# Kernel tuning notes

Measured on AMD Instinct MI355X. Metric: run time of the kernel, lower is better.

## Reference

```python
import jax, jax.numpy as jnp
import numpy as np

NUM_GROUPS = 16   # static upper bound on group ids (actual ids in [0, 12))
MIN_COUNT = 10    # min_subgroup_count


def setup_inputs() -> dict:
    key = jax.random.key(0)
    ks = jax.random.split(key, 7)
    B = 32768
    N = 16777216  # dataset_size
    probs = jax.random.uniform(ks[0], (B,), dtype=jnp.float32)
    labels = jax.random.randint(ks[1], (B,), 0, 2, dtype=jnp.int32)
    groups = jax.random.randint(ks[2], (B,), 0, 12, dtype=jnp.int32)
    indices = jax.random.randint(ks[3], (B,), 0, N, dtype=jnp.int32)
    # persistent buffers, pre-filled with valid mid-epoch state
    score_buffer = jax.random.uniform(ks[4], (N,), dtype=jnp.float32)
    label_buffer = jax.random.randint(ks[5], (N,), 0, 2, dtype=jnp.int32)
    group_buffer = jax.random.randint(ks[6], (N,), 0, 12, dtype=jnp.int32)
    return {"probs": probs, "labels": labels, "groups": groups, "indices": indices,
            "score_buffer": score_buffer, "label_buffer": label_buffer,
            "group_buffer": group_buffer}


def reference(probs, labels, groups, indices, score_buffer, label_buffer, group_buffer):
    # scatter current batch into dataset-sized buffers (functional clone + write)
    scores = score_buffer.at[indices].set(probs)
    labs = label_buffer.at[indices].set(labels)
    grps = group_buffer.at[indices].set(groups)

    valid = (~jnp.isnan(scores)) & (labs >= 0) & (grps >= 0)
    scores = jnp.where(valid, scores, 0.0)        # kill NaNs before weighted sums
    seg = jnp.where(valid, grps, 0)               # invalid rows get weight 0 anyway

    def group_var(lab_val):
        # per-group mean of scores restricted to (valid & label==lab_val),
        # then unbiased variance across groups meeting the min-count threshold
        w = (valid & (labs == lab_val)).astype(scores.dtype)
        sums = jax.ops.segment_sum(scores * w, seg, num_segments=NUM_GROUPS)
        cnts = jax.ops.segment_sum(w, seg, num_segments=NUM_GROUPS)
        avg = sums / jnp.maximum(cnts, 1.0)
        incl = (cnts >= MIN_COUNT).astype(scores.dtype)
        n = incl.sum()
        mean = (avg * incl).sum() / jnp.maximum(n, 1.0)
        var = (incl * (avg - mean) ** 2).sum() / jnp.maximum(n - 1.0, 1.0)  # ddof=1
        return var, n

    pos_var, n_pos = group_var(1)
    neg_var, n_neg = group_var(0)
    pos_ok = n_pos >= 2.0
    neg_ok = n_neg >= 2.0
    loss = jnp.where(pos_ok & neg_ok, 0.5 * (pos_var + neg_var),
                     jnp.where(pos_ok, pos_var,
                               jnp.where(neg_ok, neg_var, 0.0)))
    return loss
```

## Files before the change

kernel.cpp:

```cpp
#include <hip/hip_runtime.h>
#include <hip/hip_bf16.h>


#define TBL   65536u
#define TBLM  (TBL - 1u)
#define NGR   12
#define NBK   24
#define NCOL  25
#define NTHR  256
#define CHUNK 16384
#define ITER  (CHUNK / 4 / NTHR)
#define DEPTH 4
#define MINC  10.0

__device__ __forceinline__ unsigned hash_idx(unsigned idx) {
    return (idx * 2654435761u) & TBLM;
}

__global__ void k_vote(const int* __restrict__ indices,
                       unsigned long long* __restrict__ table,
                       unsigned* __restrict__ bitmap, int B) {
    int b = blockIdx.x * blockDim.x + threadIdx.x;
    if (b >= B) return;
    unsigned idx = (unsigned)indices[b];
    atomicOr(&bitmap[idx >> 5], 1u << (idx & 31u));
    unsigned long long key = ((unsigned long long)(idx + 1u)) << 32;
    unsigned long long val = key | (unsigned long long)(unsigned)b;
    unsigned slot = hash_idx(idx);
    for (;;) {
        unsigned long long prev = atomicCAS(&table[slot], 0ULL, val);
        if (prev == 0ULL) return;
        if ((prev >> 32) == (unsigned long long)(idx + 1u)) {
            atomicMax(&table[slot], val);
            return;
        }
        slot = (slot + 1u) & TBLM;
    }
}

__global__ void k_resolve(const unsigned long long* __restrict__ table,
                          const float* __restrict__ probs,
                          const int* __restrict__ labels,
                          const int* __restrict__ groups,
                          float4* __restrict__ tbl2) {
    int s = blockIdx.x * blockDim.x + threadIdx.x;
    unsigned long long e = table[s];
    unsigned hi = (unsigned)(e >> 32);
    float4 r = make_float4(0.f, 0.f, 0.f, 0.f);
    if (hi) {
        int b = (int)(e & 0xffffffffu);
        r.x = probs[b];
        r.y = __int_as_float(labels[b]);
        r.z = __int_as_float(groups[b]);
        r.w = __uint_as_float(hi);
    }
    tbl2[s] = r;
}

__device__ __forceinline__ void apply_ovr(int idx, float& s, int& l, int& g,
        const float4* __restrict__ tbl2) {
    unsigned slot = hash_idx((unsigned)idx);
    unsigned hi = (unsigned)idx + 1u;
    for (;;) {
        float4 r = tbl2[slot];
        if (__float_as_uint(r.w) == hi) {
            s = r.x; l = __float_as_int(r.y); g = __float_as_int(r.z);
            return;
        }
        slot = (slot + 1u) & TBLM;
    }
}

__device__ __forceinline__ void quad_p1(float* __restrict__ row,
        float4 s4, int4 l4, int4 g4, unsigned bits, int v,
        const float4* __restrict__ tbl2) {
    float ss[4] = {s4.x, s4.y, s4.z, s4.w};
    int   ll[4] = {l4.x, l4.y, l4.z, l4.w};
    int   gg[4] = {g4.x, g4.y, g4.z, g4.w};
    float val[4]; int bkt[4];
#pragma unroll
    for (int e = 0; e < 4; ++e) {
        float s = ss[e]; int l = ll[e], g = gg[e];
        if ((bits >> e) & 1u)
            apply_ovr((v << 2) + e, s, l, g, tbl2);
        bool valid = (s == s) && ((unsigned)l < 2u) && ((unsigned)g < (unsigned)NGR);
        bkt[e] = valid ? (g * 2 + l) : NBK;
        val[e] = valid ? s : 0.f;
    }
#define MRG(i, j) { bool m_ = (bkt[i] == bkt[j]); \
                    val[i] += m_ ? val[j] : 0.f;  \
                    bkt[j] = m_ ? NBK : bkt[j];   \
                    val[j] = m_ ? 0.f : val[j]; }
    MRG(0,1) MRG(0,2) MRG(0,3) MRG(1,2) MRG(1,3) MRG(2,3)
#undef MRG
    float a0 = row[bkt[0]], a1 = row[bkt[1]], a2 = row[bkt[2]], a3 = row[bkt[3]];
    row[bkt[0]] = a0 + val[0];
    row[bkt[1]] = a1 + val[1];
    row[bkt[2]] = a2 + val[2];
    row[bkt[3]] = a3 + val[3];
}

__global__ __launch_bounds__(NTHR) void k_pass1(
        const float* __restrict__ sb, const int* __restrict__ lb,
        const int* __restrict__ gb, const unsigned* __restrict__ bitmap,
        const float4* __restrict__ tbl2,
        float* __restrict__ bsum, int n, int nblk) {
    __shared__ float s_acc[NTHR * NCOL];
    int tid = threadIdx.x, blk = blockIdx.x;
    for (int i = tid; i < NTHR * NCOL; i += NTHR) s_acc[i] = 0.f;
    __syncthreads();
    float* row = &s_acc[tid * NCOL];
    int vbase = (blk * CHUNK) >> 2, nv = n >> 2;
    if (vbase + (CHUNK >> 2) <= nv) {
        int v0 = vbase + tid;
        float4 ps[DEPTH]; int4 pl[DEPTH], pg[DEPTH]; unsigned pb[DEPTH];
#pragma unroll
        for (int d = 0; d < DEPTH; ++d) {
            int v = v0 + d * NTHR;
            ps[d] = ((const float4*)sb)[v];
            pl[d] = ((const int4*)lb)[v];
            pg[d] = ((const int4*)gb)[v];
            pb[d] = bitmap[v >> 3];
        }
        unsigned sh = (unsigned)((v0 & 7) * 4);
#pragma unroll
        for (int it = 0; it < ITER; ++it) {
            int d = it & (DEPTH - 1);
            int v = v0 + it * NTHR;
            float4 s4 = ps[d]; int4 l4 = pl[d], g4 = pg[d];
            unsigned bits = pb[d] >> sh;
            if (it + DEPTH < ITER) {
                int w = v + DEPTH * NTHR;
                ps[d] = ((const float4*)sb)[w];
                pl[d] = ((const int4*)lb)[w];
                pg[d] = ((const int4*)gb)[w];
                pb[d] = bitmap[w >> 3];
            }
            asm volatile("" ::: "memory");
            quad_p1(row, s4, l4, g4, bits, v, tbl2);
        }
    } else {
        for (int it = 0; it < ITER; ++it) {
            int v = vbase + it * NTHR + tid;
            if (v >= nv) break;
            float4 s4 = ((const float4*)sb)[v];
            int4   l4 = ((const int4*)lb)[v];
            int4   g4 = ((const int4*)gb)[v];
            unsigned bits = bitmap[v >> 3] >> ((v & 7) * 4);
            quad_p1(row, s4, l4, g4, bits, v, tbl2);
        }
    }
    if (blk == nblk - 1) {
        for (int i = (nv << 2) + tid; i < n; i += NTHR) {
            float s = sb[i]; int l = lb[i], g = gb[i];
            if ((bitmap[i >> 5] >> (i & 31)) & 1u)
                apply_ovr(i, s, l, g, tbl2);
            bool valid = (s == s) && ((unsigned)l < 2u) && ((unsigned)g < (unsigned)NGR);
            int bk = valid ? (g * 2 + l) : NBK;
            row[bk] += valid ? s : 0.f;
        }
    }
    __syncthreads();
    if (tid < NBK * 8) {
        int bkt = tid >> 3, sub = tid & 7;
        float sm = 0.f;
        for (int j = 0; j < 32; ++j) sm += s_acc[(sub * 32 + j) * NCOL + bkt];
        for (int d = 4; d >= 1; d >>= 1) sm += __shfl_down(sm, d, 8);
        if (!sub) bsum[bkt * nblk + blk] = sm;
    }
}

__global__ void k_scan(const float* __restrict__ bsum,
                       float* __restrict__ bpref, int nblk) {
    __shared__ double sc[NTHR];
    int t = threadIdx.x, k = blockIdx.x;
    const float* src = bsum  + (size_t)k * nblk;
    float*       dst = bpref + (size_t)k * nblk;
    double carry = 0.0;
    for (int s0 = 0; s0 < nblk; s0 += 4 * NTHR) {
        int i0 = s0 + 4 * t;
        float x0 = (i0 + 0 < nblk) ? src[i0 + 0] : 0.f;
        float x1 = (i0 + 1 < nblk) ? src[i0 + 1] : 0.f;
        float x2 = (i0 + 2 < nblk) ? src[i0 + 2] : 0.f;
        float x3 = (i0 + 3 < nblk) ? src[i0 + 3] : 0.f;
        double p0 = (double)x0, p1 = p0 + x1, p2 = p1 + x2, tot = p2 + x3;
        sc[t] = tot;
        __syncthreads();
        for (int st = 1; st < NTHR; st <<= 1) {
            double a = (t >= st) ? sc[t - st] : 0.0;
            __syncthreads();
            sc[t] += a;
            __syncthreads();
        }
        double excl = carry + sc[t] - tot;
        if (i0 + 0 < nblk) dst[i0 + 0] = (float)excl;
        if (i0 + 1 < nblk) dst[i0 + 1] = (float)(excl + p0);
        if (i0 + 2 < nblk) dst[i0 + 2] = (float)(excl + p1);
        if (i0 + 3 < nblk) dst[i0 + 3] = (float)(excl + p2);
        double bt = sc[NTHR - 1];
        __syncthreads();
        carry += bt;
    }
}

__device__ __forceinline__ double aload_d(const double* p) {
    unsigned long long u = __hip_atomic_load((const unsigned long long*)p,
                              __ATOMIC_RELAXED, __HIP_MEMORY_SCOPE_AGENT);
    return __longlong_as_double((long long)u);
}

__device__ __forceinline__ void quad_p2(float2* __restrict__ row,
        const float2* __restrict__ s_model,
        float4 s4, int4 l4, int4 g4, unsigned bits, int v, int base,
        const float4* __restrict__ tbl2) {
    float ss[4] = {s4.x, s4.y, s4.z, s4.w};
    int   ll[4] = {l4.x, l4.y, l4.z, l4.w};
    int   gg[4] = {g4.x, g4.y, g4.z, g4.w};
    float cv[4], cn[4]; int bkt[4];
#pragma unroll
    for (int e = 0; e < 4; ++e) {
        int idx = (v << 2) + e;
        float s = ss[e]; int l = ll[e], g = gg[e];
        if ((bits >> e) & 1u)
            apply_ovr(idx, s, l, g, tbl2);
        bool valid = (s == s) && ((unsigned)l < 2u) && ((unsigned)g < (unsigned)NGR);
        int bk = valid ? (g * 2 + l) : NBK;
        float2 m = s_model[bk];
        float S = fmaf(m.y, (float)(idx - base), m.x);
        float T = S + s;
        unsigned ue = __float_as_uint(T) & 0x7f800000u;
        float c;
        if (ue < (24u << 23)) c = s;
        else {
            unsigned ub = ue - (23u << 23);
            float u    = __uint_as_float(ub);
            float uinv = __uint_as_float((254u << 23) - ub);
            c = u * rintf(s * uinv);
        }
        bkt[e] = bk;
        cv[e] = valid ? c : 0.f;
        cn[e] = valid ? 1.f : 0.f;
    }
#define MRG(i, j) { bool m_ = (bkt[i] == bkt[j]); \
                    cv[i] += m_ ? cv[j] : 0.f;    \
                    cn[i] += m_ ? cn[j] : 0.f;    \
                    bkt[j] = m_ ? NBK : bkt[j];   \
                    cv[j] = m_ ? 0.f : cv[j];     \
                    cn[j] = m_ ? 0.f : cn[j]; }
    MRG(0,1) MRG(0,2) MRG(0,3) MRG(1,2) MRG(1,3) MRG(2,3)
#undef MRG
    float2 a0 = row[bkt[0]], a1 = row[bkt[1]], a2 = row[bkt[2]], a3 = row[bkt[3]];
    a0.x += cv[0]; a0.y += cn[0];
    a1.x += cv[1]; a1.y += cn[1];
    a2.x += cv[2]; a2.y += cn[2];
    a3.x += cv[3]; a3.y += cn[3];
    row[bkt[0]] = a0; row[bkt[1]] = a1; row[bkt[2]] = a2; row[bkt[3]] = a3;
}

__global__ __launch_bounds__(NTHR) void k_pass2(
        const float* __restrict__ sb, const int* __restrict__ lb,
        const int* __restrict__ gb, const unsigned* __restrict__ bitmap,
        const float4* __restrict__ tbl2,
        const float* __restrict__ bsum, const float* __restrict__ bpref,
        double* __restrict__ acc_sum, double* __restrict__ acc_cnt,
        unsigned* __restrict__ done, float* __restrict__ out,
        int n, int nblk) {
    __shared__ float2 s_acc[NTHR * NCOL];
    __shared__ float2 s_model[NCOL];
    int tid = threadIdx.x, blk = blockIdx.x;
    for (int i = tid; i < NTHR * NCOL; i += NTHR) s_acc[i] = make_float2(0.f, 0.f);
    if (tid < NBK)
        s_model[tid] = make_float2(bpref[tid * nblk + blk],
                                   bsum[tid * nblk + blk] * (1.0f / CHUNK));
    if (tid == NBK) s_model[NBK] = make_float2(0.f, 0.f);
    __syncthreads();
    float2* row = &s_acc[tid * NCOL];
    int base = blk * CHUNK;
    int vbase = base >> 2, nv = n >> 2;
    if (vbase + (CHUNK >> 2) <= nv) {
        int v0 = vbase + tid;
        float4 ps[DEPTH]; int4 pl[DEPTH], pg[DEPTH]; unsigned pb[DEPTH];
#pragma unroll
        for (int d = 0; d < DEPTH; ++d) {
            int v = v0 + d * NTHR;
            ps[d] = ((const float4*)sb)[v];
            pl[d] = ((const int4*)lb)[v];
            pg[d] = ((const int4*)gb)[v];
            pb[d] = bitmap[v >> 3];
        }
        unsigned sh = (unsigned)((v0 & 7) * 4);
#pragma unroll
        for (int it = 0; it < ITER; ++it) {
            int d = it & (DEPTH - 1);
            int v = v0 + it * NTHR;
            float4 s4 = ps[d]; int4 l4 = pl[d], g4 = pg[d];
            unsigned bits = pb[d] >> sh;
            if (it + DEPTH < ITER) {
                int w = v + DEPTH * NTHR;
                ps[d] = ((const float4*)sb)[w];
                pl[d] = ((const int4*)lb)[w];
                pg[d] = ((const int4*)gb)[w];
                pb[d] = bitmap[w >> 3];
            }
            asm volatile("" ::: "memory");
            quad_p2(row, s_model, s4, l4, g4, bits, v, base, tbl2);
        }
    } else {
        for (int it = 0; it < ITER; ++it) {
            int v = vbase + it * NTHR + tid;
            if (v >= nv) break;
            float4 s4 = ((const float4*)sb)[v];
            int4   l4 = ((const int4*)lb)[v];
            int4   g4 = ((const int4*)gb)[v];
            unsigned bits = bitmap[v >> 3] >> ((v & 7) * 4);
            quad_p2(row, s_model, s4, l4, g4, bits, v, base, tbl2);
        }
    }
    if (blk == nblk - 1) {
        for (int i = (nv << 2) + tid; i < n; i += NTHR) {
            float s = sb[i]; int l = lb[i], g = gb[i];
            if ((bitmap[i >> 5] >> (i & 31)) & 1u)
                apply_ovr(i, s, l, g, tbl2);
            bool valid = (s == s) && ((unsigned)l < 2u) && ((unsigned)g < (unsigned)NGR);
            int bk = valid ? (g * 2 + l) : NBK;
            float2 m = s_model[bk];
            float S = fmaf(m.y, (float)(i - base), m.x);
            float T = S + s;
            unsigned ue = __float_as_uint(T) & 0x7f800000u;
            float c;
            if (ue < (24u << 23)) c = s;
            else {
                unsigned ub = ue - (23u << 23);
                float u    = __uint_as_float(ub);
                float uinv = __uint_as_float((254u << 23) - ub);
                c = u * rintf(s * uinv);
            }
            float2 a = row[bk];
            a.x += valid ? c : 0.f;
            a.y += valid ? 1.f : 0.f;
            row[bk] = a;
        }
    }
    __syncthreads();
    if (tid < NBK * 8) {
        int bkt = tid >> 3, sub = tid & 7;
        float sm = 0.f, cc = 0.f;
        for (int j = 0; j < 32; ++j) {
            float2 a = s_acc[(sub * 32 + j) * NCOL + bkt];
            sm += a.x; cc += a.y;
        }
        for (int d = 4; d >= 1; d >>= 1) {
            sm += __shfl_down(sm, d, 8);
            cc += __shfl_down(cc, d, 8);
        }
        if (!sub) {
            atomicAdd(&acc_sum[bkt], (double)sm);
            atomicAdd(&acc_cnt[bkt], (double)cc);
        }
    }
    __syncthreads();
    if (tid == 0) {
        __threadfence();
        unsigned r = __hip_atomic_fetch_add(done, 1u, __ATOMIC_ACQ_REL,
                                            __HIP_MEMORY_SCOPE_AGENT);
        if (r == (unsigned)(gridDim.x - 1)) {
            double var[2], nn[2];
            for (int l = 0; l < 2; ++l) {
                double avg[NGR];
                double ncnt = 0.0, s = 0.0;
                for (int g = 0; g < NGR; ++g) {
                    double c  = aload_d(&acc_cnt[g * 2 + l]);
                    double sm = aload_d(&acc_sum[g * 2 + l]);
                    double a = sm / fmax(c, 1.0);
                    avg[g] = a;
                    if (c >= MINC) { ncnt += 1.0; s += a; }
                }
                double mean = s / fmax(ncnt, 1.0), v = 0.0;
                for (int g = 0; g < NGR; ++g) {
                    double c = aload_d(&acc_cnt[g * 2 + l]);
                    if (c >= MINC) { double d = avg[g] - mean; v += d * d; }
                }
                var[l] = v / fmax(ncnt - 1.0, 1.0);
                nn[l] = ncnt;
            }
            bool p = nn[1] >= 2.0, q = nn[0] >= 2.0;
            double loss = (p && q) ? 0.5 * (var[1] + var[0])
                        : (p ? var[1] : (q ? var[0] : 0.0));
            out[0] = (float)loss;
        }
    }
}

extern "C" void kernel_launch(void* const* d_in, const int* in_sizes, int n_in,
                              void* d_out, int out_size, void* d_ws, size_t ws_size,
                              hipStream_t stream) {
    const float* probs   = (const float*)d_in[0];
    const int*   labels  = (const int*)d_in[1];
    const int*   groups  = (const int*)d_in[2];
    const int*   indices = (const int*)d_in[3];
    const float* sb      = (const float*)d_in[4];
    const int*   lb      = (const int*)d_in[5];
    const int*   gb      = (const int*)d_in[6];
    int B = in_sizes[0];
    int n = in_sizes[4];
    int nblk   = (n + CHUNK - 1) / CHUNK;
    int nwords = (n + 31) / 32;

    char* ws = (char*)d_ws;
    size_t off = 0;
    unsigned long long* table = (unsigned long long*)(ws + off); off += (size_t)TBL * 8;
    unsigned* bitmap  = (unsigned*)(ws + off); off += (size_t)nwords * 4;
    double*   acc_sum = (double*)(ws + off);   off += NBK * 8;
    double*   acc_cnt = (double*)(ws + off);   off += NBK * 8;
    unsigned* done    = (unsigned*)(ws + off); off += 8;
    size_t zero_bytes = off;
    float4*   tbl2    = (float4*)(ws + off);   off += (size_t)TBL * 16;
    float*    bsum    = (float*)(ws + off);    off += (size_t)nblk * NBK * 4;
    float*    bpref   = (float*)(ws + off);    off += (size_t)nblk * NBK * 4;

    hipMemsetAsync(d_ws, 0, zero_bytes, stream);

    dim3 bblk((B + NTHR - 1) / NTHR);
    hipLaunchKernelGGL(k_vote, bblk, dim3(NTHR), 0, stream,
                       indices, table, bitmap, B);
    hipLaunchKernelGGL(k_resolve, dim3(TBL / NTHR), dim3(NTHR), 0, stream,
                       table, probs, labels, groups, tbl2);
    hipLaunchKernelGGL(k_pass1, dim3(nblk), dim3(NTHR), 0, stream,
                       sb, lb, gb, bitmap, tbl2, bsum, n, nblk);
    hipLaunchKernelGGL(k_scan, dim3(NBK), dim3(NTHR), 0, stream,
                       bsum, bpref, nblk);
    hipLaunchKernelGGL(k_pass2, dim3(nblk), dim3(NTHR), 0, stream,
                       sb, lb, gb, bitmap, tbl2, bsum, bpref,
                       acc_sum, acc_cnt, done, (float*)d_out, n, nblk);
}
```

Measured before the change: 334.7 us.

## Fuse prefix scan into pass1 tail and move counts from pass2 to pass1

```diff
diff --git a/kernel.cpp b/kernel.cpp
--- a/kernel.cpp
+++ b/kernel.cpp
@@ -8,9 +8,11 @@
 #define NBK   24
 #define NCOL  25
 #define NTHR  256
+#define NW    (NTHR / 64)
 #define CHUNK 16384
 #define ITER  (CHUNK / 4 / NTHR)
 #define DEPTH 4
+#define GRP   4
 #define MINC  10.0
 
 __device__ __forceinline__ unsigned hash_idx(unsigned idx) {
@@ -71,26 +73,49 @@
     }
 }
 
+__device__ __forceinline__ float aload_f(const float* p) {
+    unsigned u = __hip_atomic_load((const unsigned*)p,
+                     __ATOMIC_RELAXED, __HIP_MEMORY_SCOPE_AGENT);
+    return __uint_as_float(u);
+}
+__device__ __forceinline__ void astore_f(float* p, float v) {
+    __hip_atomic_store((unsigned*)p, __float_as_uint(v),
+                       __ATOMIC_RELAXED, __HIP_MEMORY_SCOPE_AGENT);
+}
+__device__ __forceinline__ double aload_d(const double* p) {
+    unsigned long long u = __hip_atomic_load((const unsigned long long*)p,
+                              __ATOMIC_RELAXED, __HIP_MEMORY_SCOPE_AGENT);
+    return __longlong_as_double((long long)u);
+}
+
 __device__ __forceinline__ void quad_p1(float* __restrict__ row,
+        unsigned* __restrict__ cntw,
         float4 s4, int4 l4, int4 g4, unsigned bits, int v,
         const float4* __restrict__ tbl2) {
     float ss[4] = {s4.x, s4.y, s4.z, s4.w};
     int   ll[4] = {l4.x, l4.y, l4.z, l4.w};
     int   gg[4] = {g4.x, g4.y, g4.z, g4.w};
-    float val[4]; int bkt[4];
+    if (bits & 0xFu) {
+#pragma unroll
+        for (int e = 0; e < 4; ++e)
+            if ((bits >> e) & 1u)
+                apply_ovr((v << 2) + e, ss[e], ll[e], gg[e], tbl2);
+    }
+    float val[4]; int bkt[4], cn[4];
 #pragma unroll
     for (int e = 0; e < 4; ++e) {
-        float s = ss[e]; int l = ll[e], g = gg[e];
-        if ((bits >> e) & 1u)
-            apply_ovr((v << 2) + e, s, l, g, tbl2);
-        bool valid = (s == s) && ((unsigned)l < 2u) && ((unsigned)g < (unsigned)NGR);
-        bkt[e] = valid ? (g * 2 + l) : NBK;
-        val[e] = valid ? s : 0.f;
+        bool valid = (ss[e] == ss[e]) && ((unsigned)ll[e] < 2u) &&
+                     ((unsigned)gg[e] < (unsigned)NGR);
+        bkt[e] = valid ? (gg[e] * 2 + ll[e]) : NBK;
+        val[e] = valid ? ss[e] : 0.f;
+        cn[e]  = valid ? 1 : 0;
     }
 #define MRG(i, j) { bool m_ = (bkt[i] == bkt[j]); \
                     val[i] += m_ ? val[j] : 0.f;  \
+                    cn[i]  += m_ ? cn[j] : 0;     \
                     bkt[j] = m_ ? NBK : bkt[j];   \
-                    val[j] = m_ ? 0.f : val[j]; }
+                    val[j] = m_ ? 0.f : val[j];   \
+                    cn[j]  = m_ ? 0 : cn[j]; }
     MRG(0,1) MRG(0,2) MRG(0,3) MRG(1,2) MRG(1,3) MRG(2,3)
 #undef MRG
     float a0 = row[bkt[0]], a1 = row[bkt[1]], a2 = row[bkt[2]], a3 = row[bkt[3]];
@@ -98,18 +123,32 @@
     row[bkt[1]] = a1 + val[1];
     row[bkt[2]] = a2 + val[2];
     row[bkt[3]] = a3 + val[3];
+    atomicAdd(&cntw[bkt[0]], (unsigned)cn[0]);
+    atomicAdd(&cntw[bkt[1]], (unsigned)cn[1]);
+    atomicAdd(&cntw[bkt[2]], (unsigned)cn[2]);
+    atomicAdd(&cntw[bkt[3]], (unsigned)cn[3]);
 }
 
 __global__ __launch_bounds__(NTHR) void k_pass1(
         const float* __restrict__ sb, const int* __restrict__ lb,
         const int* __restrict__ gb, const unsigned* __restrict__ bitmap,
         const float4* __restrict__ tbl2,
-        float* __restrict__ bsum, int n, int nblk) {
-    __shared__ float s_acc[NTHR * NCOL];
+        float* __restrict__ bsum, float* __restrict__ bpref,
+        double* __restrict__ acc_cnt, unsigned* __restrict__ done1,
+        int n, int nblk) {
+    __shared__ __align__(16) float s_acc[NTHR * NCOL];
+    __shared__ unsigned s_cnt[NW * NCOL];
+    __shared__ unsigned s_last;
     int tid = threadIdx.x, blk = blockIdx.x;
     for (int i = tid; i < NTHR * NCOL; i += NTHR) s_acc[i] = 0.f;
-    __syncthreads();
+    if (tid < NW * NCOL) s_cnt[tid] = 0u;
+    __syncthreads();
+    int wv = tid >> 6;
+    if (wv == 1) __builtin_amdgcn_s_sleep(4);
+    else if (wv == 2) __builtin_amdgcn_s_sleep(7);
+    else if (wv == 3) __builtin_amdgcn_s_sleep(10);
     float* row = &s_acc[tid * NCOL];
+    unsigned* cntw = &s_cnt[wv * NCOL];
     int vbase = (blk * CHUNK) >> 2, nv = n >> 2;
     if (vbase + (CHUNK >> 2) <= nv) {
         int v0 = vbase + tid;
@@ -137,7 +176,7 @@
                 pb[d] = bitmap[w >> 3];
             }
             asm volatile("" ::: "memory");
-            quad_p1(row, s4, l4, g4, bits, v, tbl2);
+            quad_p1(row, cntw, s4, l4, g4, bits, v, tbl2);
         }
     } else {
         for (int it = 0; it < ITER; ++it) {
@@ -147,7 +186,7 @@
             int4   l4 = ((const int4*)lb)[v];
             int4   g4 = ((const int4*)gb)[v];
             unsigned bits = bitmap[v >> 3] >> ((v & 7) * 4);
-            quad_p1(row, s4, l4, g4, bits, v, tbl2);
+            quad_p1(row, cntw, s4, l4, g4, bits, v, tbl2);
         }
     }
     if (blk == nblk - 1) {
@@ -158,6 +197,7 @@
             bool valid = (s == s) && ((unsigned)l < 2u) && ((unsigned)g < (unsigned)NGR);
             int bk = valid ? (g * 2 + l) : NBK;
             row[bk] += valid ? s : 0.f;
+            atomicAdd(&cntw[bk], valid ? 1u : 0u);
         }
     }
     __syncthreads();
@@ -166,65 +206,90 @@
         float sm = 0.f;
         for (int j = 0; j < 32; ++j) sm += s_acc[(sub * 32 + j) * NCOL + bkt];
         for (int d = 4; d >= 1; d >>= 1) sm += __shfl_down(sm, d, 8);
-        if (!sub) bsum[bkt * nblk + blk] = sm;
-    }
-}
-
-__global__ void k_scan(const float* __restrict__ bsum,
-                       float* __restrict__ bpref, int nblk) {
-    __shared__ double sc[NTHR];
-    int t = threadIdx.x, k = blockIdx.x;
-    const float* src = bsum  + (size_t)k * nblk;
-    float*       dst = bpref + (size_t)k * nblk;
-    double carry = 0.0;
-    for (int s0 = 0; s0 < nblk; s0 += 4 * NTHR) {
-        int i0 = s0 + 4 * t;
-        float x0 = (i0 + 0 < nblk) ? src[i0 + 0] : 0.f;
-        float x1 = (i0 + 1 < nblk) ? src[i0 + 1] : 0.f;
-        float x2 = (i0 + 2 < nblk) ? src[i0 + 2] : 0.f;
-        float x3 = (i0 + 3 < nblk) ? src[i0 + 3] : 0.f;
-        double p0 = (double)x0, p1 = p0 + x1, p2 = p1 + x2, tot = p2 + x3;
-        sc[t] = tot;
-        __syncthreads();
-        for (int st = 1; st < NTHR; st <<= 1) {
-            double a = (t >= st) ? sc[t - st] : 0.0;
+        if (!sub) astore_f(&bsum[bkt * nblk + blk], sm);
+    }
+    if (tid < NBK) {
+        unsigned tot = 0;
+#pragma unroll
+        for (int w = 0; w < NW; ++w) tot += s_cnt[w * NCOL + tid];
+        if (tot) atomicAdd(&acc_cnt[tid], (double)tot);
+    }
+    __syncthreads();
+    if (tid == 0) {
+        __threadfence();
+        unsigned r = __hip_atomic_fetch_add(done1, 1u, __ATOMIC_ACQ_REL,
+                                            __HIP_MEMORY_SCOPE_AGENT);
+        s_last = (r == (unsigned)(gridDim.x - 1)) ? 1u : 0u;
+    }
+    __syncthreads();
+    if (!s_last) return;
+    double* sc2 = (double*)s_acc;
+    int t = tid;
+    for (int k0 = 0; k0 < NBK; k0 += GRP) {
+        double carry[GRP];
+#pragma unroll
+        for (int q = 0; q < GRP; ++q) carry[q] = 0.0;
+        for (int s0 = 0; s0 < nblk; s0 += 4 * NTHR) {
+            int i0 = s0 + 4 * t;
+            double p0[GRP], p1[GRP], p2[GRP], tt[GRP];
+#pragma unroll
+            for (int q = 0; q < GRP; ++q) {
+                const float* src = bsum + (size_t)(k0 + q) * nblk;
+                float x0 = (i0 + 0 < nblk) ? aload_f(src + i0 + 0) : 0.f;
+                float x1 = (i0 + 1 < nblk) ? aload_f(src + i0 + 1) : 0.f;
+                float x2 = (i0 + 2 < nblk) ? aload_f(src + i0 + 2) : 0.f;
+                float x3 = (i0 + 3 < nblk) ? aload_f(src + i0 + 3) : 0.f;
+                p0[q] = (double)x0; p1[q] = p0[q] + x1;
+                p2[q] = p1[q] + x2; tt[q] = p2[q] + x3;
+                sc2[q * NTHR + t] = tt[q];
+            }
             __syncthreads();
-            sc[t] += a;
+            for (int st = 1; st < NTHR; st <<= 1) {
+                double a[GRP];
+#pragma unroll
+                for (int q = 0; q < GRP; ++q)
+                    a[q] = (t >= st) ? sc2[q * NTHR + t - st] : 0.0;
+                __syncthreads();
+#pragma unroll
+                for (int q = 0; q < GRP; ++q) sc2[q * NTHR + t] += a[q];
+                __syncthreads();
+            }
+#pragma unroll
+            for (int q = 0; q < GRP; ++q) {
+                double excl = carry[q] + sc2[q * NTHR + t] - tt[q];
+                float* dst = bpref + (size_t)(k0 + q) * nblk;
+                if (i0 + 0 < nblk) dst[i0 + 0] = (float)excl;
+                if (i0 + 1 < nblk) dst[i0 + 1] = (float)(excl + p0[q]);
+                if (i0 + 2 < nblk) dst[i0 + 2] = (float)(excl + p1[q]);
+                if (i0 + 3 < nblk) dst[i0 + 3] = (float)(excl + p2[q]);
+                carry[q] += sc2[q * NTHR + NTHR - 1];
+            }
             __syncthreads();
         }
-        double excl = carry + sc[t] - tot;
-        if (i0 + 0 < nblk) dst[i0 + 0] = (float)excl;
-        if (i0 + 1 < nblk) dst[i0 + 1] = (float)(excl + p0);
-        if (i0 + 2 < nblk) dst[i0 + 2] = (float)(excl + p1);
-        if (i0 + 3 < nblk) dst[i0 + 3] = (float)(excl + p2);
-        double bt = sc[NTHR - 1];
-        __syncthreads();
-        carry += bt;
-    }
-}
-
-__device__ __forceinline__ double aload_d(const double* p) {
-    unsigned long long u = __hip_atomic_load((const unsigned long long*)p,
-                              __ATOMIC_RELAXED, __HIP_MEMORY_SCOPE_AGENT);
-    return __longlong_as_double((long long)u);
-}
-
-__device__ __forceinline__ void quad_p2(float2* __restrict__ row,
+    }
+}
+
+__device__ __forceinline__ void quad_p2(float* __restrict__ row,
         const float2* __restrict__ s_model,
         float4 s4, int4 l4, int4 g4, unsigned bits, int v, int base,
         const float4* __restrict__ tbl2) {
     float ss[4] = {s4.x, s4.y, s4.z, s4.w};
     int   ll[4] = {l4.x, l4.y, l4.z, l4.w};
     int   gg[4] = {g4.x, g4.y, g4.z, g4.w};
-    float cv[4], cn[4]; int bkt[4];
+    if (bits & 0xFu) {
+#pragma unroll
+        for (int e = 0; e < 4; ++e)
+            if ((bits >> e) & 1u)
+                apply_ovr((v << 2) + e, ss[e], ll[e], gg[e], tbl2);
+    }
+    float cv[4]; int bkt[4];
 #pragma unroll
     for (int e = 0; e < 4; ++e) {
         int idx = (v << 2) + e;
-        float s = ss[e]; int l = ll[e], g = gg[e];
-        if ((bits >> e) & 1u)
-            apply_ovr(idx, s, l, g, tbl2);
-        bool valid = (s == s) && ((unsigned)l < 2u) && ((unsigned)g < (unsigned)NGR);
-        int bk = valid ? (g * 2 + l) : NBK;
+        float s = ss[e];
+        bool valid = (s == s) && ((unsigned)ll[e] < 2u) &&
+                     ((unsigned)gg[e] < (unsigned)NGR);
+        int bk = valid ? (gg[e] * 2 + ll[e]) : NBK;
         float2 m = s_model[bk];
         float S = fmaf(m.y, (float)(idx - base), m.x);
         float T = S + s;
@@ -239,22 +304,18 @@
         }
         bkt[e] = bk;
         cv[e] = valid ? c : 0.f;
-        cn[e] = valid ? 1.f : 0.f;
     }
 #define MRG(i, j) { bool m_ = (bkt[i] == bkt[j]); \
                     cv[i] += m_ ? cv[j] : 0.f;    \
-                    cn[i] += m_ ? cn[j] : 0.f;    \
                     bkt[j] = m_ ? NBK : bkt[j];   \
-                    cv[j] = m_ ? 0.f : cv[j];     \
-                    cn[j] = m_ ? 0.f : cn[j]; }
+                    cv[j] = m_ ? 0.f : cv[j]; }
     MRG(0,1) MRG(0,2) MRG(0,3) MRG(1,2) MRG(1,3) MRG(2,3)
 #undef MRG
-    float2 a0 = row[bkt[0]], a1 = row[bkt[1]], a2 = row[bkt[2]], a3 = row[bkt[3]];
-    a0.x += cv[0]; a0.y += cn[0];
-    a1.x += cv[1]; a1.y += cn[1];
-    a2.x += cv[2]; a2.y += cn[2];
-    a3.x += cv[3]; a3.y += cn[3];
-    row[bkt[0]] = a0; row[bkt[1]] = a1; row[bkt[2]] = a2; row[bkt[3]] = a3;
+    float a0 = row[bkt[0]], a1 = row[bkt[1]], a2 = row[bkt[2]], a3 = row[bkt[3]];
+    row[bkt[0]] = a0 + cv[0];
+    row[bkt[1]] = a1 + cv[1];
+    row[bkt[2]] = a2 + cv[2];
+    row[bkt[3]] = a3 + cv[3];
 }
 
 __global__ __launch_bounds__(NTHR) void k_pass2(
@@ -263,18 +324,22 @@
         const float4* __restrict__ tbl2,
         const float* __restrict__ bsum, const float* __restrict__ bpref,
         double* __restrict__ acc_sum, double* __restrict__ acc_cnt,
-        unsigned* __restrict__ done, float* __restrict__ out,
+        unsigned* __restrict__ done2, float* __restrict__ out,
         int n, int nblk) {
-    __shared__ float2 s_acc[NTHR * NCOL];
+    __shared__ float s_acc[NTHR * NCOL];
     __shared__ float2 s_model[NCOL];
     int tid = threadIdx.x, blk = blockIdx.x;
-    for (int i = tid; i < NTHR * NCOL; i += NTHR) s_acc[i] = make_float2(0.f, 0.f);
+    for (int i = tid; i < NTHR * NCOL; i += NTHR) s_acc[i] = 0.f;
     if (tid < NBK)
         s_model[tid] = make_float2(bpref[tid * nblk + blk],
                                    bsum[tid * nblk + blk] * (1.0f / CHUNK));
     if (tid == NBK) s_model[NBK] = make_float2(0.f, 0.f);
     __syncthreads();
-    float2* row = &s_acc[tid * NCOL];
+    int wv = tid >> 6;
+    if (wv == 1) __builtin_amdgcn_s_sleep(4);
+    else if (wv == 2) __builtin_amdgcn_s_sleep(7);
+    else if (wv == 3) __builtin_amdgcn_s_sleep(10);
+    float* row = &s_acc[tid * NCOL];
     int base = blk * CHUNK;
     int vbase = base >> 2, nv = n >> 2;
     if (vbase + (CHUNK >> 2) <= nv) {
@@ -335,33 +400,21 @@
                 float uinv = __uint_as_float((254u << 23) - ub);
                 c = u * rintf(s * uinv);
             }
-            float2 a = row[bk];
-            a.x += valid ? c : 0.f;
-            a.y += valid ? 1.f : 0.f;
-            row[bk] = a;
+            row[bk] += valid ? c : 0.f;
         }
     }
     __syncthreads();
     if (tid < NBK * 8) {
         int bkt = tid >> 3, sub = tid & 7;
-        float sm = 0.f, cc = 0.f;
-        for (int j = 0; j < 32; ++j) {
-            float2 a = s_acc[(sub * 32 + j) * NCOL + bkt];
-            sm += a.x; cc += a.y;
-        }
-        for (int d = 4; d >= 1; d >>= 1) {
-            sm += __shfl_down(sm, d, 8);
-            cc += __shfl_down(cc, d, 8);
-        }
-        if (!sub) {
-            atomicAdd(&acc_sum[bkt], (double)sm);
-            atomicAdd(&acc_cnt[bkt], (double)cc);
-        }
+        float sm = 0.f;
+        for (int j = 0; j < 32; ++j) sm += s_acc[(sub * 32 + j) * NCOL + bkt];
+        for (int d = 4; d >= 1; d >>= 1) sm += __shfl_down(sm, d, 8);
+        if (!sub) atomicAdd(&acc_sum[bkt], (double)sm);
     }
     __syncthreads();
     if (tid == 0) {
         __threadfence();
-        unsigned r = __hip_atomic_fetch_add(done, 1u, __ATOMIC_ACQ_REL,
+        unsigned r = __hip_atomic_fetch_add(done2, 1u, __ATOMIC_ACQ_REL,
                                             __HIP_MEMORY_SCOPE_AGENT);
         if (r == (unsigned)(gridDim.x - 1)) {
             double var[2], nn[2];
@@ -410,9 +463,10 @@
     size_t off = 0;
     unsigned long long* table = (unsigned long long*)(ws + off); off += (size_t)TBL * 8;
     unsigned* bitmap  = (unsigned*)(ws + off); off += (size_t)nwords * 4;
+    off = (off + 15) & ~(size_t)15;
     double*   acc_sum = (double*)(ws + off);   off += NBK * 8;
     double*   acc_cnt = (double*)(ws + off);   off += NBK * 8;
-    unsigned* done    = (unsigned*)(ws + off); off += 8;
+    unsigned* done    = (unsigned*)(ws + off); off += 16;
     size_t zero_bytes = off;
     float4*   tbl2    = (float4*)(ws + off);   off += (size_t)TBL * 16;
     float*    bsum    = (float*)(ws + off);    off += (size_t)nblk * NBK * 4;
@@ -426,10 +480,9 @@
     hipLaunchKernelGGL(k_resolve, dim3(TBL / NTHR), dim3(NTHR), 0, stream,
                        table, probs, labels, groups, tbl2);
     hipLaunchKernelGGL(k_pass1, dim3(nblk), dim3(NTHR), 0, stream,
-                       sb, lb, gb, bitmap, tbl2, bsum, n, nblk);
-    hipLaunchKernelGGL(k_scan, dim3(NBK), dim3(NTHR), 0, stream,
-                       bsum, bpref, nblk);
+                       sb, lb, gb, bitmap, tbl2, bsum, bpref,
+                       acc_cnt, done + 0, n, nblk);
     hipLaunchKernelGGL(k_pass2, dim3(nblk), dim3(NTHR), 0, stream,
                        sb, lb, gb, bitmap, tbl2, bsum, bpref,
-                       acc_sum, acc_cnt, done, (float*)d_out, n, nblk);
-}
+                       acc_sum, acc_cnt, done + 1, (float*)d_out, n, nblk);
+}
```

After: 380.5 us. 13.7% more time.

## Cache per-element bucket ids in pass1 so pass2 skips label/group reads

Applied to the files above, without the earlier changes.

```diff
diff --git a/kernel.cpp b/kernel.cpp
--- a/kernel.cpp
+++ b/kernel.cpp
@@ -10,7 +10,8 @@
 #define NTHR  256
 #define CHUNK 16384
 #define ITER  (CHUNK / 4 / NTHR)
-#define DEPTH 4
+#define DEPTH1 4
+#define DEPTH2 8
 #define MINC  10.0
 
 __device__ __forceinline__ unsigned hash_idx(unsigned idx) {
@@ -71,22 +72,40 @@
     }
 }
 
+__device__ __forceinline__ float ovr_s(int idx,
+        const float4* __restrict__ tbl2) {
+    unsigned slot = hash_idx((unsigned)idx);
+    unsigned hi = (unsigned)idx + 1u;
+    for (;;) {
+        float4 r = tbl2[slot];
+        if (__float_as_uint(r.w) == hi) return r.x;
+        slot = (slot + 1u) & TBLM;
+    }
+}
+
 __device__ __forceinline__ void quad_p1(float* __restrict__ row,
+        unsigned* __restrict__ bstr32,
         float4 s4, int4 l4, int4 g4, unsigned bits, int v,
         const float4* __restrict__ tbl2) {
     float ss[4] = {s4.x, s4.y, s4.z, s4.w};
     int   ll[4] = {l4.x, l4.y, l4.z, l4.w};
     int   gg[4] = {g4.x, g4.y, g4.z, g4.w};
+    if (bits & 0xFu) {
+#pragma unroll
+        for (int e = 0; e < 4; ++e)
+            if ((bits >> e) & 1u)
+                apply_ovr((v << 2) + e, ss[e], ll[e], gg[e], tbl2);
+    }
     float val[4]; int bkt[4];
 #pragma unroll
     for (int e = 0; e < 4; ++e) {
-        float s = ss[e]; int l = ll[e], g = gg[e];
-        if ((bits >> e) & 1u)
-            apply_ovr((v << 2) + e, s, l, g, tbl2);
-        bool valid = (s == s) && ((unsigned)l < 2u) && ((unsigned)g < (unsigned)NGR);
-        bkt[e] = valid ? (g * 2 + l) : NBK;
-        val[e] = valid ? s : 0.f;
-    }
+        bool valid = (ss[e] == ss[e]) && ((unsigned)ll[e] < 2u) &&
+                     ((unsigned)gg[e] < (unsigned)NGR);
+        bkt[e] = valid ? (gg[e] * 2 + ll[e]) : NBK;
+        val[e] = valid ? ss[e] : 0.f;
+    }
+    bstr32[v] = (unsigned)bkt[0] | ((unsigned)bkt[1] << 8) |
+                ((unsigned)bkt[2] << 16) | ((unsigned)bkt[3] << 24);
 #define MRG(i, j) { bool m_ = (bkt[i] == bkt[j]); \
                     val[i] += m_ ? val[j] : 0.f;  \
                     bkt[j] = m_ ? NBK : bkt[j];   \
@@ -104,18 +123,20 @@
         const float* __restrict__ sb, const int* __restrict__ lb,
         const int* __restrict__ gb, const unsigned* __restrict__ bitmap,
         const float4* __restrict__ tbl2,
-        float* __restrict__ bsum, int n, int nblk) {
+        float* __restrict__ bsum, unsigned char* __restrict__ bstream,
+        int n, int nblk) {
     __shared__ float s_acc[NTHR * NCOL];
     int tid = threadIdx.x, blk = blockIdx.x;
     for (int i = tid; i < NTHR * NCOL; i += NTHR) s_acc[i] = 0.f;
     __syncthreads();
     float* row = &s_acc[tid * NCOL];
+    unsigned* bstr32 = (unsigned*)bstream;
     int vbase = (blk * CHUNK) >> 2, nv = n >> 2;
     if (vbase + (CHUNK >> 2) <= nv) {
         int v0 = vbase + tid;
-        float4 ps[DEPTH]; int4 pl[DEPTH], pg[DEPTH]; unsigned pb[DEPTH];
-#pragma unroll
-        for (int d = 0; d < DEPTH; ++d) {
+        float4 ps[DEPTH1]; int4 pl[DEPTH1], pg[DEPTH1]; unsigned pb[DEPTH1];
+#pragma unroll
+        for (int d = 0; d < DEPTH1; ++d) {
             int v = v0 + d * NTHR;
             ps[d] = ((const float4*)sb)[v];
             pl[d] = ((const int4*)lb)[v];
@@ -125,19 +146,19 @@
         unsigned sh = (unsigned)((v0 & 7) * 4);
 #pragma unroll
         for (int it = 0; it < ITER; ++it) {
-            int d = it & (DEPTH - 1);
+            int d = it & (DEPTH1 - 1);
             int v = v0 + it * NTHR;
             float4 s4 = ps[d]; int4 l4 = pl[d], g4 = pg[d];
             unsigned bits = pb[d] >> sh;
-            if (it + DEPTH < ITER) {
-                int w = v + DEPTH * NTHR;
+            if (it + DEPTH1 < ITER) {
+                int w = v + DEPTH1 * NTHR;
                 ps[d] = ((const float4*)sb)[w];
                 pl[d] = ((const int4*)lb)[w];
                 pg[d] = ((const int4*)gb)[w];
                 pb[d] = bitmap[w >> 3];
             }
             asm volatile("" ::: "memory");
-            quad_p1(row, s4, l4, g4, bits, v, tbl2);
+            quad_p1(row, bstr32, s4, l4, g4, bits, v, tbl2);
         }
     } else {
         for (int it = 0; it < ITER; ++it) {
@@ -147,7 +168,7 @@
             int4   l4 = ((const int4*)lb)[v];
             int4   g4 = ((const int4*)gb)[v];
             unsigned bits = bitmap[v >> 3] >> ((v & 7) * 4);
-            quad_p1(row, s4, l4, g4, bits, v, tbl2);
+            quad_p1(row, bstr32, s4, l4, g4, bits, v, tbl2);
         }
     }
     if (blk == nblk - 1) {
@@ -157,6 +178,7 @@
                 apply_ovr(i, s, l, g, tbl2);
             bool valid = (s == s) && ((unsigned)l < 2u) && ((unsigned)g < (unsigned)NGR);
             int bk = valid ? (g * 2 + l) : NBK;
+            bstream[i] = (unsigned char)bk;
             row[bk] += valid ? s : 0.f;
         }
     }
@@ -211,20 +233,20 @@
 
 __device__ __forceinline__ void quad_p2(float2* __restrict__ row,
         const float2* __restrict__ s_model,
-        float4 s4, int4 l4, int4 g4, unsigned bits, int v, int base,
+        float4 s4, unsigned b4, unsigned obits, int v, int base,
         const float4* __restrict__ tbl2) {
     float ss[4] = {s4.x, s4.y, s4.z, s4.w};
-    int   ll[4] = {l4.x, l4.y, l4.z, l4.w};
-    int   gg[4] = {g4.x, g4.y, g4.z, g4.w};
+    if (obits & 0xFu) {
+#pragma unroll
+        for (int e = 0; e < 4; ++e)
+            if ((obits >> e) & 1u) ss[e] = ovr_s((v << 2) + e, tbl2);
+    }
     float cv[4], cn[4]; int bkt[4];
 #pragma unroll
     for (int e = 0; e < 4; ++e) {
         int idx = (v << 2) + e;
-        float s = ss[e]; int l = ll[e], g = gg[e];
-        if ((bits >> e) & 1u)
-            apply_ovr(idx, s, l, g, tbl2);
-        bool valid = (s == s) && ((unsigned)l < 2u) && ((unsigned)g < (unsigned)NGR);
-        int bk = valid ? (g * 2 + l) : NBK;
+        int bk = (int)((b4 >> (8 * e)) & 0xFFu);
+        float s = ss[e];
         float2 m = s_model[bk];
         float S = fmaf(m.y, (float)(idx - base), m.x);
         float T = S + s;
@@ -237,6 +259,7 @@
             float uinv = __uint_as_float((254u << 23) - ub);
             c = u * rintf(s * uinv);
         }
+        bool valid = bk < NBK;
         bkt[e] = bk;
         cv[e] = valid ? c : 0.f;
         cn[e] = valid ? 1.f : 0.f;
@@ -258,8 +281,9 @@
 }
 
 __global__ __launch_bounds__(NTHR) void k_pass2(
-        const float* __restrict__ sb, const int* __restrict__ lb,
-        const int* __restrict__ gb, const unsigned* __restrict__ bitmap,
+        const float* __restrict__ sb,
+        const unsigned char* __restrict__ bstream,
+        const unsigned* __restrict__ bitmap,
         const float4* __restrict__ tbl2,
         const float* __restrict__ bsum, const float* __restrict__ bpref,
         double* __restrict__ acc_sum, double* __restrict__ acc_cnt,
@@ -275,54 +299,51 @@
     if (tid == NBK) s_model[NBK] = make_float2(0.f, 0.f);
     __syncthreads();
     float2* row = &s_acc[tid * NCOL];
+    const unsigned* bstr32 = (const unsigned*)bstream;
     int base = blk * CHUNK;
     int vbase = base >> 2, nv = n >> 2;
     if (vbase + (CHUNK >> 2) <= nv) {
         int v0 = vbase + tid;
-        float4 ps[DEPTH]; int4 pl[DEPTH], pg[DEPTH]; unsigned pb[DEPTH];
-#pragma unroll
-        for (int d = 0; d < DEPTH; ++d) {
+        float4 ps[DEPTH2]; unsigned pk[DEPTH2], pb[DEPTH2];
+#pragma unroll
+        for (int d = 0; d < DEPTH2; ++d) {
             int v = v0 + d * NTHR;
             ps[d] = ((const float4*)sb)[v];
-            pl[d] = ((const int4*)lb)[v];
-            pg[d] = ((const int4*)gb)[v];
+            pk[d] = bstr32[v];
             pb[d] = bitmap[v >> 3];
         }
         unsigned sh = (unsigned)((v0 & 7) * 4);
 #pragma unroll
         for (int it = 0; it < ITER; ++it) {
-            int d = it & (DEPTH - 1);
+            int d = it & (DEPTH2 - 1);
             int v = v0 + it * NTHR;
-            float4 s4 = ps[d]; int4 l4 = pl[d], g4 = pg[d];
+            float4 s4 = ps[d]; unsigned b4 = pk[d];
             unsigned bits = pb[d] >> sh;
-            if (it + DEPTH < ITER) {
-                int w = v + DEPTH * NTHR;
+            if (it + DEPTH2 < ITER) {
+                int w = v + DEPTH2 * NTHR;
                 ps[d] = ((const float4*)sb)[w];
-                pl[d] = ((const int4*)lb)[w];
-                pg[d] = ((const int4*)gb)[w];
+                pk[d] = bstr32[w];
                 pb[d] = bitmap[w >> 3];
             }
             asm volatile("" ::: "memory");
-            quad_p2(row, s_model, s4, l4, g4, bits, v, base, tbl2);
+            quad_p2(row, s_model, s4, b4, bits, v, base, tbl2);
         }
     } else {
         for (int it = 0; it < ITER; ++it) {
             int v = vbase + it * NTHR + tid;
             if (v >= nv) break;
             float4 s4 = ((const float4*)sb)[v];
-            int4   l4 = ((const int4*)lb)[v];
-            int4   g4 = ((const int4*)gb)[v];
+            unsigned b4 = bstr32[v];
             unsigned bits = bitmap[v >> 3] >> ((v & 7) * 4);
-            quad_p2(row, s_model, s4, l4, g4, bits, v, base, tbl2);
+            quad_p2(row, s_model, s4, b4, bits, v, base, tbl2);
         }
     }
     if (blk == nblk - 1) {
         for (int i = (nv << 2) + tid; i < n; i += NTHR) {
-            float s = sb[i]; int l = lb[i], g = gb[i];
+            float s = sb[i];
+            int bk = (int)bstream[i];
             if ((bitmap[i >> 5] >> (i & 31)) & 1u)
-                apply_ovr(i, s, l, g, tbl2);
-            bool valid = (s == s) && ((unsigned)l < 2u) && ((unsigned)g < (unsigned)NGR);
-            int bk = valid ? (g * 2 + l) : NBK;
+                s = ovr_s(i, tbl2);
             float2 m = s_model[bk];
             float S = fmaf(m.y, (float)(i - base), m.x);
             float T = S + s;
@@ -335,6 +356,7 @@
                 float uinv = __uint_as_float((254u << 23) - ub);
                 c = u * rintf(s * uinv);
             }
+            bool valid = bk < NBK;
             float2 a = row[bk];
             a.x += valid ? c : 0.f;
             a.y += valid ? 1.f : 0.f;
@@ -410,11 +432,14 @@
     size_t off = 0;
     unsigned long long* table = (unsigned long long*)(ws + off); off += (size_t)TBL * 8;
     unsigned* bitmap  = (unsigned*)(ws + off); off += (size_t)nwords * 4;
+    off = (off + 15) & ~(size_t)15;
     double*   acc_sum = (double*)(ws + off);   off += NBK * 8;
     double*   acc_cnt = (double*)(ws + off);   off += NBK * 8;
-    unsigned* done    = (unsigned*)(ws + off); off += 8;
+    unsigned* done    = (unsigned*)(ws + off); off += 16;
     size_t zero_bytes = off;
     float4*   tbl2    = (float4*)(ws + off);   off += (size_t)TBL * 16;
+    unsigned char* bstream = (unsigned char*)(ws + off);
+    off += ((size_t)n + 15) & ~(size_t)15;
     float*    bsum    = (float*)(ws + off);    off += (size_t)nblk * NBK * 4;
     float*    bpref   = (float*)(ws + off);    off += (size_t)nblk * NBK * 4;
 
@@ -426,10 +451,10 @@
     hipLaunchKernelGGL(k_resolve, dim3(TBL / NTHR), dim3(NTHR), 0, stream,
                        table, probs, labels, groups, tbl2);
     hipLaunchKernelGGL(k_pass1, dim3(nblk), dim3(NTHR), 0, stream,
-                       sb, lb, gb, bitmap, tbl2, bsum, n, nblk);
+                       sb, lb, gb, bitmap, tbl2, bsum, bstream, n, nblk);
     hipLaunchKernelGGL(k_scan, dim3(NBK), dim3(NTHR), 0, stream,
                        bsum, bpref, nblk);
     hipLaunchKernelGGL(k_pass2, dim3(nblk), dim3(NTHR), 0, stream,
-                       sb, lb, gb, bitmap, tbl2, bsum, bpref,
+                       sb, bstream, bitmap, tbl2, bsum, bpref,
                        acc_sum, acc_cnt, done, (float*)d_out, n, nblk);
 }
```

Result: faster. 325.7 us (-2.7%).
